# Kernel tuning notes

Hardware: AMD Instinct MI355X
Metric: run time of the kernel (lower is better)

Reference implementation:

```python
import jax, jax.numpy as jnp
import numpy as np

DIM = 1024
NUM_HEADS = 16
HEAD_DIM = DIM // NUM_HEADS
SCALE = HEAD_DIM ** -0.5


def setup_inputs() -> dict:
    key = jax.random.key(0)
    ks = jax.random.split(key, 7)
    s = DIM ** -0.5
    return {
        "x": jax.random.normal(ks[0], (4, 2048, DIM), dtype=jnp.float32),
        "wq": jax.random.normal(ks[1], (DIM, DIM), dtype=jnp.float32) * s,
        "wk": jax.random.normal(ks[2], (DIM, DIM), dtype=jnp.float32) * s,
        "wv": jax.random.normal(ks[3], (DIM, DIM), dtype=jnp.float32) * s,
        "wo": jax.random.normal(ks[4], (DIM, DIM), dtype=jnp.float32) * s,
        "bo": jax.random.normal(ks[5], (DIM,), dtype=jnp.float32) * 0.02,
    }


def reference(x, wq, wk, wv, wo, bo):
    B, N, C = x.shape
    H, D = NUM_HEADS, HEAD_DIM
    # projections (qkv_bias=False); weights stored as [out, in] like nn.Linear
    q = jnp.einsum("bnc,oc->bno", x, wq).reshape(B, N, H, D).transpose(0, 2, 1, 3)
    k = jnp.einsum("bnc,oc->bno", x, wk).reshape(B, N, H, D).transpose(0, 2, 1, 3)
    v = jnp.einsum("bnc,oc->bno", x, wv).reshape(B, N, H, D).transpose(0, 2, 1, 3)
    # full NxN scores, scaled after the matmul as in the original
    scores = jnp.einsum("bhqd,bhkd->bhqk", q, k) * SCALE
    probs = jax.nn.softmax(scores, axis=-1)  # attn_drop is identity (p=0, eval)
    out = jnp.einsum("bhqk,bhkd->bhqd", probs, v)
    out = out.transpose(0, 2, 1, 3).reshape(B, N, C)
    # output projection with bias; proj_drop identity
    return jnp.einsum("bnc,oc->bno", out, wo) + bo
```

## Files before the change

kernel.cpp:

```cpp
#include <hip/hip_runtime.h>

typedef unsigned short u16;
typedef __attribute__((ext_vector_type(8))) short short8;
typedef __attribute__((ext_vector_type(4))) float f32x4;

#define LOG2E 1.44269504088896340736f

__device__ __forceinline__ u16 f2bf(float f) {
    unsigned u = __float_as_uint(f);
    u += 0x7fffu + ((u >> 16) & 1u);
    return (u16)(u >> 16);
}

__device__ __forceinline__ void async_cp16(const void* g, void* l) {
    __builtin_amdgcn_global_load_lds(
        (const __attribute__((address_space(1))) unsigned*)g,
        (__attribute__((address_space(3))) unsigned*)l, 16, 0, 0);
}

__device__ __forceinline__ unsigned pack_trunc(float a, float b) {
    return __builtin_amdgcn_perm(__float_as_uint(b), __float_as_uint(a), 0x07060302u);
}

__global__ void cast_all(const float4* __restrict__ x,
                         const float4* __restrict__ wq, const float4* __restrict__ wk,
                         const float4* __restrict__ wv, const float4* __restrict__ wo,
                         uint2* __restrict__ xb, uint2* __restrict__ wqkv,
                         uint2* __restrict__ wob) {
    long long g = (long long)blockIdx.x * blockDim.x + threadIdx.x;
    const long long XG = (8192LL * 1024) / 4;
    const long long WN = (1024LL * 1024) / 4;
    float4 v;
    uint2* dst;
    if (g < XG) {
        v = x[g];
        dst = xb + g;
    } else {
        long long t = g - XG;
        int s = (int)(t / WN);
        long long r = t - (long long)s * WN;
        const float4* src = (s == 0) ? wq : (s == 1) ? wk : (s == 2) ? wv : wo;
        v = src[r];
        dst = (s < 3) ? (wqkv + (long long)s * WN + r) : (wob + r);
    }
    uint2 p;
    p.x = (unsigned)f2bf(v.x) | ((unsigned)f2bf(v.y) << 16);
    p.y = (unsigned)f2bf(v.z) | ((unsigned)f2bf(v.w) << 16);
    *dst = p;
}

template <int MODE>
__global__ __launch_bounds__(256, 2) void gemm_nt(
    const u16* __restrict__ A, const u16* __restrict__ Bw,
    u16* __restrict__ Qo, u16* __restrict__ Ko, u16* __restrict__ Vto,
    float* __restrict__ Fo, const float* __restrict__ bias, int K) {
    __shared__ u16 As[128 * 64];
    __shared__ u16 Bs[128 * 64];

    const int tid = threadIdx.x;
    const int lane = tid & 63, wave = tid >> 6;
    const int wm = wave >> 1, wn = wave & 1;
    const int quad = lane >> 4, l16 = lane & 15;
    const long long m0 = (long long)blockIdx.x * 128;
    const long long n0 = (long long)blockIdx.y * 128;

    f32x4 acc[4][4];
#pragma unroll
    for (int i = 0; i < 4; i++)
#pragma unroll
        for (int j = 0; j < 4; j++) acc[i][j] = (f32x4){0.f, 0.f, 0.f, 0.f};

    for (int kt = 0; kt < K; kt += 64) {
#pragma unroll
        for (int i = 0; i < 4; i++) {
            int ff = i * 256 + tid;
            int row = ff >> 3, c = ff & 7;
            int gc = c ^ (row & 7);
            async_cp16(A + (m0 + row) * K + kt + gc * 8, &As[ff * 8]);
            async_cp16(Bw + (n0 + row) * K + kt + gc * 8, &Bs[ff * 8]);
        }
        __syncthreads();
#pragma unroll
        for (int ks = 0; ks < 2; ks++) {
            short8 af[4], bfr[4];
#pragma unroll
            for (int t = 0; t < 4; t++) {
                int rowA = wm * 64 + t * 16 + l16;
                int ca = (ks * 4 + quad) ^ (rowA & 7);
                af[t] = *(const short8*)(&As[rowA * 64 + ca * 8]);
                int rowB = wn * 64 + t * 16 + l16;
                int cb = (ks * 4 + quad) ^ (rowB & 7);
                bfr[t] = *(const short8*)(&Bs[rowB * 64 + cb * 8]);
            }
#pragma unroll
            for (int i = 0; i < 4; i++)
#pragma unroll
                for (int j = 0; j < 4; j++)
                    acc[i][j] = __builtin_amdgcn_mfma_f32_16x16x32_bf16(
                        af[i], bfr[j], acc[i][j], 0, 0, 0);
        }
        __syncthreads();
    }

#pragma unroll
    for (int i = 0; i < 4; i++) {
        int mg = (int)m0 + wm * 64 + i * 16 + quad * 4;
#pragma unroll
        for (int j = 0; j < 4; j++) {
            int ng = (int)n0 + wn * 64 + j * 16 + l16;
            f32x4 v = acc[i][j];
            if (MODE == 0) {
                int which = ng >> 10;
                int wi = ng & 1023;
                int h = wi >> 6, d = wi & 63;
                int b = mg >> 11;
                int seq = mg & 2047;
                long long bh = (long long)(b * 16 + h);
                if (which == 0) {
                    const float QS = 0.125f * LOG2E;
                    u16* dst = Qo + (bh * 2048 + seq) * 64 + d;
#pragma unroll
                    for (int r = 0; r < 4; r++) dst[r * 64] = f2bf(v[r] * QS);
                } else if (which == 1) {
                    u16* dst = Ko + (bh * 2048 + seq) * 64 + d;
#pragma unroll
                    for (int r = 0; r < 4; r++) dst[r * 64] = f2bf(v[r]);
                } else {
                    u16* dst = Vto + (bh * 64 + d) * 2048 + seq;
                    uint2 p;
                    p.x = (unsigned)f2bf(v[0]) | ((unsigned)f2bf(v[1]) << 16);
                    p.y = (unsigned)f2bf(v[2]) | ((unsigned)f2bf(v[3]) << 16);
                    *(uint2*)dst = p;
                }
            } else {
                float* dst = Fo + (long long)mg * 1024 + ng;
                float bb = bias[ng];
#pragma unroll
                for (int r = 0; r < 4; r++) dst[r * 1024] = v[r] + bb;
            }
        }
    }
}

__global__ __launch_bounds__(512, 4) void attn(
    const u16* __restrict__ Q, const u16* __restrict__ Kb,
    const u16* __restrict__ Vt, u16* __restrict__ O) {
    __shared__ u16 Ks[2][64 * 64];
    __shared__ u16 Vs[2][64 * 64];
    __shared__ u16 Ps[8][32 * 64];

    const int tid = threadIdx.x;
    const int lane = tid & 63, wave = tid >> 6;
    const int quad = lane >> 4, l16 = lane & 15;
    const int bh = blockIdx.x, qt = blockIdx.y;

    const u16* Qh = Q + (long long)bh * 2048 * 64;
    const u16* Kh = Kb + (long long)bh * 2048 * 64;
    const u16* Vh = Vt + (long long)bh * 64 * 2048;
    const int q0 = qt * 256 + wave * 32;

    const int srow = tid >> 3, sc = tid & 7;
    const int sgc = sc ^ (srow & 7);
    const u16* Kg = Kh + srow * 64 + sgc * 8;
    const u16* Vg = Vh + (long long)srow * 2048 + sgc * 8;

    short8 qf[2][2];
#pragma unroll
    for (int tm = 0; tm < 2; tm++)
#pragma unroll
        for (int ks = 0; ks < 2; ks++)
            qf[tm][ks] = *(const short8*)(Qh + (q0 + tm * 16 + l16) * 64 + ks * 32 + quad * 8);

    u16* Pw = &Ps[wave][0];
    int pwr[2][4], prd[2][2], kvo[2][4];
#pragma unroll
    for (int tm = 0; tm < 2; tm++) {
        const int qrow = tm * 16 + l16;
#pragma unroll
        for (int tn = 0; tn < 4; tn++)
            pwr[tm][tn] = qrow * 64 + (((tn * 2 + (quad >> 1)) ^ (l16 & 7)) * 8) + 4 * (quad & 1);
#pragma unroll
        for (int ks = 0; ks < 2; ks++)
            prd[tm][ks] = qrow * 64 + (((ks * 4 + quad) ^ (l16 & 7)) * 8);
    }
#pragma unroll
    for (int ks = 0; ks < 2; ks++)
#pragma unroll
        for (int tn = 0; tn < 4; tn++) {
            int row = tn * 16 + l16;
            kvo[ks][tn] = row * 64 + (((ks * 4 + quad) ^ (row & 7)) * 8);
        }

    f32x4 o_acc[2][4], lacc[2];
#pragma unroll
    for (int tm = 0; tm < 2; tm++) {
        lacc[tm] = (f32x4){0.f, 0.f, 0.f, 0.f};
#pragma unroll
        for (int tn = 0; tn < 4; tn++) o_acc[tm][tn] = (f32x4){0.f, 0.f, 0.f, 0.f};
    }
    const float NEGC = -12.0f * LOG2E;
    const short BF1 = (short)0x3F80;
    const short8 ones = {BF1, BF1, BF1, BF1, BF1, BF1, BF1, BF1};

    async_cp16(Kg, &Ks[0][tid * 8]);
    async_cp16(Vg, &Vs[0][tid * 8]);

#define ATTN_STEP(KT, BUF)                                                              \
    do {                                                                                \
        __syncthreads();                                                                \
        if ((KT) < 31) {                                                                \
            async_cp16(Kg + ((KT) + 1) * 4096, &Ks[(BUF) ^ 1][tid * 8]);                \
            async_cp16(Vg + ((KT) + 1) * 64, &Vs[(BUF) ^ 1][tid * 8]);                  \
        }                                                                               \
        const u16* Kc = &Ks[BUF][0];                                                    \
        const u16* Vc = &Vs[BUF][0];                                                    \
        f32x4 s[2][4];                                                                  \
        _Pragma("unroll") for (int tm = 0; tm < 2; tm++)                                \
            _Pragma("unroll") for (int tn = 0; tn < 4; tn++)                            \
                s[tm][tn] = (f32x4){NEGC, NEGC, NEGC, NEGC};                            \
        _Pragma("unroll") for (int ks = 0; ks < 2; ks++) {                              \
            short8 kf[4];                                                               \
            _Pragma("unroll") for (int tn = 0; tn < 4; tn++)                            \
                kf[tn] = *(const short8*)(&Kc[kvo[ks][tn]]);                            \
            _Pragma("unroll") for (int tm = 0; tm < 2; tm++)                            \
                _Pragma("unroll") for (int tn = 0; tn < 4; tn++)                        \
                    s[tm][tn] = __builtin_amdgcn_mfma_f32_16x16x32_bf16(                \
                        kf[tn], qf[tm][ks], s[tm][tn], 0, 0, 0);                        \
        }                                                                               \
        _Pragma("unroll") for (int tm = 0; tm < 2; tm++)                                \
            _Pragma("unroll") for (int tn = 0; tn < 4; tn++) {                          \
                f32x4 sv = s[tm][tn];                                                   \
                float p0 = __builtin_amdgcn_exp2f(sv[0]);                               \
                float p1 = __builtin_amdgcn_exp2f(sv[1]);                               \
                float p2 = __builtin_amdgcn_exp2f(sv[2]);                               \
                float p3 = __builtin_amdgcn_exp2f(sv[3]);                               \
                uint2 pk;                                                               \
                pk.x = pack_trunc(p0, p1);                                              \
                pk.y = pack_trunc(p2, p3);                                              \
                *(uint2*)(&Pw[pwr[tm][tn]]) = pk;                                       \
            }                                                                           \
        _Pragma("unroll") for (int ks = 0; ks < 2; ks++) {                              \
            short8 vf[4];                                                               \
            _Pragma("unroll") for (int tn = 0; tn < 4; tn++)                            \
                vf[tn] = *(const short8*)(&Vc[kvo[ks][tn]]);                            \
            short8 pf0 = *(const short8*)(&Pw[prd[0][ks]]);                             \
            short8 pf1 = *(const short8*)(&Pw[prd[1][ks]]);                             \
            lacc[0] = __builtin_amdgcn_mfma_f32_16x16x32_bf16(pf0, ones, lacc[0], 0, 0, 0); \
            lacc[1] = __builtin_amdgcn_mfma_f32_16x16x32_bf16(pf1, ones, lacc[1], 0, 0, 0); \
            _Pragma("unroll") for (int tn = 0; tn < 4; tn++) {                          \
                o_acc[0][tn] = __builtin_amdgcn_mfma_f32_16x16x32_bf16(                 \
                    pf0, vf[tn], o_acc[0][tn], 0, 0, 0);                                \
                o_acc[1][tn] = __builtin_amdgcn_mfma_f32_16x16x32_bf16(                 \
                    pf1, vf[tn], o_acc[1][tn], 0, 0, 0);                                \
            }                                                                           \
        }                                                                               \
    } while (0)

#pragma unroll 1
    for (int kt = 0; kt < 32; kt += 2) {
        ATTN_STEP(kt, 0);
        ATTN_STEP(kt + 1, 1);
    }
#undef ATTN_STEP

    f32x4 linv[2];
#pragma unroll
    for (int tm = 0; tm < 2; tm++)
#pragma unroll
        for (int r = 0; r < 4; r++) linv[tm][r] = 1.0f / lacc[tm][r];

    const int b = bh >> 4, h = bh & 15;
#pragma unroll
    for (int tm = 0; tm < 2; tm++)
#pragma unroll
        for (int tn = 0; tn < 4; tn++) {
            int seq = q0 + tm * 16 + quad * 4;
            int c = h * 64 + tn * 16 + l16;
            u16* dst = O + ((long long)(b * 2048 + seq)) * 1024 + c;
#pragma unroll
            for (int r = 0; r < 4; r++)
                dst[r * 1024] = f2bf(o_acc[tm][tn][r] * linv[tm][r]);
        }
}

extern "C" void kernel_launch(void* const* d_in, const int* in_sizes, int n_in,
                              void* d_out, int out_size, void* d_ws, size_t ws_size,
                              hipStream_t stream) {
    const float* x = (const float*)d_in[0];
    const float* wq = (const float*)d_in[1];
    const float* wk = (const float*)d_in[2];
    const float* wv = (const float*)d_in[3];
    const float* wo = (const float*)d_in[4];
    const float* bo = (const float*)d_in[5];
    float* out = (float*)d_out;

    char* ws = (char*)d_ws;
    u16* xb   = (u16*)(ws);
    u16* wqkv = (u16*)(ws + (16LL << 20));
    u16* wob  = (u16*)(ws + (22LL << 20));
    u16* Qb   = (u16*)(ws + (24LL << 20));
    u16* Kbuf = (u16*)(ws + (40LL << 20));
    u16* Vt   = (u16*)(ws + (56LL << 20));
    u16* Ob   = (u16*)(ws + (72LL << 20));

    cast_all<<<12288, 256, 0, stream>>>((const float4*)x, (const float4*)wq,
                                        (const float4*)wk, (const float4*)wv,
                                        (const float4*)wo, (uint2*)xb,
                                        (uint2*)wqkv, (uint2*)wob);

    dim3 g1(64, 24);
    gemm_nt<0><<<g1, 256, 0, stream>>>(xb, wqkv, Qb, Kbuf, Vt, nullptr, nullptr, 1024);

    dim3 g2(64, 8);
    attn<<<g2, 512, 0, stream>>>(Qb, Kbuf, Vt, Ob);

    dim3 g3(64, 8);
    gemm_nt<1><<<g3, 256, 0, stream>>>(Ob, wob, nullptr, nullptr, nullptr, out, bo, 1024);
}
```

Measured before the change: 249.0 us.

## Load V fragments directly from global, halve attention block size, swizzle GEMM tiles

The attention kernel stops staging V through LDS and instead loads each wave's V^T fragments straight from global memory into registers. The LDS freed this way now double-buffers K, with each thread copying two chunks per tile. Blocks shrink from 512 to 256 threads (128 queries each) and the grid doubles, reducing LDS per block so more blocks can be resident. The projection GEMMs switch to a 1D grid with a block-index remap that groups M-tiles under the same N-tile for better L2 reuse. The trade-off is redundant global/L2 reads of V across waves and exposed global load latency inside the loop.

```diff
diff --git a/kernel.cpp b/kernel.cpp
--- a/kernel.cpp
+++ b/kernel.cpp
@@ -61,8 +61,12 @@
     const int lane = tid & 63, wave = tid >> 6;
     const int wm = wave >> 1, wn = wave & 1;
     const int quad = lane >> 4, l16 = lane & 15;
-    const long long m0 = (long long)blockIdx.x * 128;
-    const long long n0 = (long long)blockIdx.y * 128;
+    const int bid = blockIdx.x;
+    const int gg = bid >> 3;
+    const int mt = (bid & 7) * 8 + (gg & 7);
+    const int nt = gg >> 3;
+    const long long m0 = (long long)mt * 128;
+    const long long n0 = (long long)nt * 128;
 
     f32x4 acc[4][4];
 #pragma unroll
@@ -142,12 +146,11 @@
     }
 }
 
-__global__ __launch_bounds__(512, 4) void attn(
+__global__ __launch_bounds__(256, 4) void attn(
     const u16* __restrict__ Q, const u16* __restrict__ Kb,
     const u16* __restrict__ Vt, u16* __restrict__ O) {
     __shared__ u16 Ks[2][64 * 64];
-    __shared__ u16 Vs[2][64 * 64];
-    __shared__ u16 Ps[8][32 * 64];
+    __shared__ u16 Ps[4][32 * 64];
 
     const int tid = threadIdx.x;
     const int lane = tid & 63, wave = tid >> 6;
@@ -157,12 +160,16 @@
     const u16* Qh = Q + (long long)bh * 2048 * 64;
     const u16* Kh = Kb + (long long)bh * 2048 * 64;
     const u16* Vh = Vt + (long long)bh * 64 * 2048;
-    const int q0 = qt * 256 + wave * 32;
+    const int q0 = qt * 128 + wave * 32;
 
     const int srow = tid >> 3, sc = tid & 7;
     const int sgc = sc ^ (srow & 7);
     const u16* Kg = Kh + srow * 64 + sgc * 8;
-    const u16* Vg = Vh + (long long)srow * 2048 + sgc * 8;
+
+    const u16* vb[4];
+#pragma unroll
+    for (int tn = 0; tn < 4; tn++)
+        vb[tn] = Vh + (long long)(tn * 16 + l16) * 2048 + quad * 8;
 
     short8 qf[2][2];
 #pragma unroll
@@ -203,17 +210,21 @@
     const short8 ones = {BF1, BF1, BF1, BF1, BF1, BF1, BF1, BF1};
 
     async_cp16(Kg, &Ks[0][tid * 8]);
-    async_cp16(Vg, &Vs[0][tid * 8]);
+    async_cp16(Kg + 2048, &Ks[0][tid * 8 + 2048]);
 
 #define ATTN_STEP(KT, BUF)                                                              \
     do {                                                                                \
         __syncthreads();                                                                \
         if ((KT) < 31) {                                                                \
             async_cp16(Kg + ((KT) + 1) * 4096, &Ks[(BUF) ^ 1][tid * 8]);                \
-            async_cp16(Vg + ((KT) + 1) * 64, &Vs[(BUF) ^ 1][tid * 8]);                  \
+            async_cp16(Kg + ((KT) + 1) * 4096 + 2048, &Ks[(BUF) ^ 1][tid * 8 + 2048]);  \
         }                                                                               \
+                      \
+        short8 vf[2][4];                                                                \
+        _Pragma("unroll") for (int ks = 0; ks < 2; ks++)                                \
+            _Pragma("unroll") for (int tn = 0; tn < 4; tn++)                            \
+                vf[ks][tn] = *(const short8*)(vb[tn] + (KT) * 64 + ks * 32);            \
         const u16* Kc = &Ks[BUF][0];                                                    \
-        const u16* Vc = &Vs[BUF][0];                                                    \
         f32x4 s[2][4];                                                                  \
         _Pragma("unroll") for (int tm = 0; tm < 2; tm++)                                \
             _Pragma("unroll") for (int tn = 0; tn < 4; tn++)                            \
@@ -240,18 +251,15 @@
                 *(uint2*)(&Pw[pwr[tm][tn]]) = pk;                                       \
             }                                                                           \
         _Pragma("unroll") for (int ks = 0; ks < 2; ks++) {                              \
-            short8 vf[4];                                                               \
-            _Pragma("unroll") for (int tn = 0; tn < 4; tn++)                            \
-                vf[tn] = *(const short8*)(&Vc[kvo[ks][tn]]);                            \
             short8 pf0 = *(const short8*)(&Pw[prd[0][ks]]);                             \
             short8 pf1 = *(const short8*)(&Pw[prd[1][ks]]);                             \
             lacc[0] = __builtin_amdgcn_mfma_f32_16x16x32_bf16(pf0, ones, lacc[0], 0, 0, 0); \
             lacc[1] = __builtin_amdgcn_mfma_f32_16x16x32_bf16(pf1, ones, lacc[1], 0, 0, 0); \
             _Pragma("unroll") for (int tn = 0; tn < 4; tn++) {                          \
                 o_acc[0][tn] = __builtin_amdgcn_mfma_f32_16x16x32_bf16(                 \
-                    pf0, vf[tn], o_acc[0][tn], 0, 0, 0);                                \
+                    pf0, vf[ks][tn], o_acc[0][tn], 0, 0, 0);                            \
                 o_acc[1][tn] = __builtin_amdgcn_mfma_f32_16x16x32_bf16(                 \
-                    pf1, vf[tn], o_acc[1][tn], 0, 0, 0);                                \
+                    pf1, vf[ks][tn], o_acc[1][tn], 0, 0, 0);                            \
             }                                                                           \
         }                                                                               \
     } while (0)
@@ -308,12 +316,10 @@
                                         (const float4*)wo, (uint2*)xb,
                                         (uint2*)wqkv, (uint2*)wob);
 
-    dim3 g1(64, 24);
-    gemm_nt<0><<<g1, 256, 0, stream>>>(xb, wqkv, Qb, Kbuf, Vt, nullptr, nullptr, 1024);
-
-    dim3 g2(64, 8);
-    attn<<<g2, 512, 0, stream>>>(Qb, Kbuf, Vt, Ob);
-
-    dim3 g3(64, 8);
-    gemm_nt<1><<<g3, 256, 0, stream>>>(Ob, wob, nullptr, nullptr, nullptr, out, bo, 1024);
-}
+    gemm_nt<0><<<64 * 24, 256, 0, stream>>>(xb, wqkv, Qb, Kbuf, Vt, nullptr, nullptr, 1024);
+
+    dim3 g2(64, 16);
+    attn<<<g2, 256, 0, stream>>>(Qb, Kbuf, Vt, Ob);
+
+    gemm_nt<1><<<64 * 8, 256, 0, stream>>>(Ob, wob, nullptr, nullptr, nullptr, out, bo, 1024);
+}
```

Result: slower. 305.8 us (+22.8%).
